# Optimization experiments

Measured on AMD Instinct MI355X. Metric: run time of the kernel, lower is better.

## Reference

```python
import jax, jax.numpy as jnp
import numpy as np

DIM = 64
N_EMBED = 512


def setup_inputs() -> dict:
    key = jax.random.key(0)
    k_x, k_e = jax.random.split(key)
    x = jax.random.normal(k_x, (32, 64, 64, DIM), dtype=jnp.float32)
    # codebook buffer: embed has shape [dim, n_embed] as in the torch module
    embed = jax.random.normal(k_e, (DIM, N_EMBED), dtype=jnp.float32)
    return {"x": x, "embed": embed}


def reference(x, embed):
    # x: [B, H, W, dim]; embed: [dim, n_embed]
    dim = embed.shape[0]
    flat = x.reshape(-1, dim)  # [N, dim]
    # squared euclidean distance (same argmin as torch.cdist's euclid dist)
    # d2[n, k] = ||flat[n]||^2 - 2 flat[n].embed[:,k] + ||embed[:,k]||^2
    d2 = (
        jnp.sum(flat * flat, axis=1, keepdims=True)
        - 2.0 * (flat @ embed)
        + jnp.sum(embed * embed, axis=0)[None, :]
    )  # [N, n_embed]
    embed_ind = jnp.argmin(d2, axis=1)  # [N]
    embed_ind = embed_ind.reshape(x.shape[:-1])  # [B, H, W]
    # embedding lookup from embed.T ([n_embed, dim])
    quantize = jnp.take(embed.T, embed_ind, axis=0)  # [B, H, W, dim]
    diff = jnp.mean(jnp.square(jax.lax.stop_gradient(quantize) - x))
    # straight-through estimator
    quantize_st = x + jax.lax.stop_gradient(quantize - x)
    return quantize_st, diff, embed_ind
```

## Files before the change

kernel.cpp:

```cpp
#include <hip/hip_runtime.h>


#define DIM      64
#define NCODE    512
#define NVEC     (32 * 64 * 64)
#define WAVES    4
#define BLK      256
#define NCT      16
#define CHUNK_DW 3072

typedef unsigned int u32;
typedef __attribute__((ext_vector_type(8)))  short bf16x8;
typedef __attribute__((ext_vector_type(16))) float f32x16;

__device__ __forceinline__ void split3(float v, u32& h, u32& m, u32& lo) {
    const u32 u = __float_as_uint(v);
    h = u >> 16;
    const float r1 = v - __uint_as_float(u & 0xFFFF0000u);
    const u32 u1 = __float_as_uint(r1);
    m = u1 >> 16;
    const float r2 = r1 - __uint_as_float(u1 & 0xFFFF0000u);
    lo = __float_as_uint(r2) >> 16;
}

__global__ void vq_prep(const float* __restrict__ embed,
                        u32* __restrict__ bfrag,
                        float* __restrict__ et,
                        float* __restrict__ norms,
                        float* __restrict__ out) {
    const int gid = blockIdx.x * BLK + threadIdx.x;
    const int c = gid >> 3, g = gid & 7;
    const int s = g >> 1, kh = g & 1;

    float v[8];
    double ns = 0.0;
    #pragma unroll
    for (int j = 0; j < 8; ++j) {
        v[j] = embed[(16 * s + 8 * kh + j) * NCODE + c];
        ns += (double)v[j] * (double)v[j];
    }
    ns += __shfl_xor(ns, 1, 64);
    ns += __shfl_xor(ns, 2, 64);
    ns += __shfl_xor(ns, 4, 64);
    if (g == 0) norms[c] = (float)ns;

    u32 wH[4], wM[4], wL[4];
    #pragma unroll
    for (int q = 0; q < 4; ++q) {
        u32 h0, m0, l0, h1, m1, l1;
        split3(v[2 * q],     h0, m0, l0);
        split3(v[2 * q + 1], h1, m1, l1);
        wH[q] = h0 | (h1 << 16);
        wM[q] = m0 | (m1 << 16);
        wL[q] = l0 | (l1 << 16);
    }
    const int ct = c >> 5, lb = (c & 31) + 32 * kh;
    u32* base = bfrag + ct * CHUNK_DW;
    *reinterpret_cast<uint4*>(base + (0 * 4 + s) * 256 + lb * 4) =
        make_uint4(wH[0], wH[1], wH[2], wH[3]);
    *reinterpret_cast<uint4*>(base + (1 * 4 + s) * 256 + lb * 4) =
        make_uint4(wM[0], wM[1], wM[2], wM[3]);
    *reinterpret_cast<uint4*>(base + (2 * 4 + s) * 256 + lb * 4) =
        make_uint4(wL[0], wL[1], wL[2], wL[3]);

    float* ep = et + c * DIM + 16 * s + 8 * kh;
    *reinterpret_cast<float4*>(ep)     = make_float4(v[0], v[1], v[2], v[3]);
    *reinterpret_cast<float4*>(ep + 4) = make_float4(v[4], v[5], v[6], v[7]);

    if (gid == 0) out[(size_t)NVEC * DIM] = 0.0f;
}

__global__ __launch_bounds__(BLK, 3) void vq_main(
        const float* __restrict__ x,
        const u32* __restrict__ bfrag,
        const float* __restrict__ et,
        const float* __restrict__ norms,
        float* __restrict__ out) {
    __shared__ int sbk[WAVES][32];
    __shared__ float red[WAVES];

    const int tid = threadIdx.x;
    const int wid = tid >> 6, l = tid & 63;
    const int rl = l & 31, kh = l >> 5;
    const int n0 = (blockIdx.x * WAVES + wid) * 32;

    bf16x8 afr[3][4];
    {
        const float* xp = x + (size_t)(n0 + rl) * DIM + kh * 8;
        #pragma unroll
        for (int s = 0; s < 4; ++s) {
            const float4 va = *reinterpret_cast<const float4*>(xp + 16 * s);
            const float4 vb = *reinterpret_cast<const float4*>(xp + 16 * s + 4);
            const float v[8] = {va.x, va.y, va.z, va.w, vb.x, vb.y, vb.z, vb.w};
            #pragma unroll
            for (int q = 0; q < 4; ++q) {
                u32 h0, m0, l0, h1, m1, l1;
                split3(v[2 * q],     h0, m0, l0);
                split3(v[2 * q + 1], h1, m1, l1);
                afr[0][s][2 * q] = (short)h0;  afr[0][s][2 * q + 1] = (short)h1;
                afr[1][s][2 * q] = (short)m0;  afr[1][s][2 * q + 1] = (short)m1;
                afr[2][s][2 * q] = (short)l0;  afr[2][s][2 * q + 1] = (short)l1;
            }
        }
    }

    float best[16];
    int bk[16];
    #pragma unroll
    for (int r = 0; r < 16; ++r) { best[r] = __builtin_inff(); bk[r] = 0; }

    const u32* fb = bfrag + (l << 2);
    for (int ct = 0; ct < NCT; ++ct) {
        const u32* tb = fb + ct * CHUNK_DW;
        bf16x8 b[3][4];
        #pragma unroll
        for (int s = 0; s < 4; ++s) {
            b[0][s] = *reinterpret_cast<const bf16x8*>(tb + (0 * 4 + s) * 256);
            b[1][s] = *reinterpret_cast<const bf16x8*>(tb + (1 * 4 + s) * 256);
            b[2][s] = *reinterpret_cast<const bf16x8*>(tb + (2 * 4 + s) * 256);
        }
        const float nrm = norms[ct * 32 + rl];

        f32x16 acc;
        #pragma unroll
        for (int r = 0; r < 16; ++r) acc[r] = 0.0f;

        #pragma unroll
        for (int s = 0; s < 4; ++s) {
            acc = __builtin_amdgcn_mfma_f32_32x32x16_bf16(afr[0][s], b[0][s], acc, 0, 0, 0);
            acc = __builtin_amdgcn_mfma_f32_32x32x16_bf16(afr[0][s], b[1][s], acc, 0, 0, 0);
            acc = __builtin_amdgcn_mfma_f32_32x32x16_bf16(afr[1][s], b[0][s], acc, 0, 0, 0);
            acc = __builtin_amdgcn_mfma_f32_32x32x16_bf16(afr[1][s], b[1][s], acc, 0, 0, 0);
            acc = __builtin_amdgcn_mfma_f32_32x32x16_bf16(afr[0][s], b[2][s], acc, 0, 0, 0);
            acc = __builtin_amdgcn_mfma_f32_32x32x16_bf16(afr[2][s], b[0][s], acc, 0, 0, 0);
        }

        const int col = ct * 32 + rl;
        #pragma unroll
        for (int r = 0; r < 16; ++r) {
            const float sc = fmaf(-2.0f, acc[r], nrm);
            if (sc < best[r]) { best[r] = sc; bk[r] = col; }
        }
    }

    #pragma unroll
    for (int off = 1; off <= 16; off <<= 1) {
        #pragma unroll
        for (int r = 0; r < 16; ++r) {
            const float ob = __shfl_xor(best[r], off, 64);
            const int obk  = __shfl_xor(bk[r], off, 64);
            if (ob < best[r] || (ob == best[r] && obk < bk[r])) { best[r] = ob; bk[r] = obk; }
        }
    }
    if (rl == 0) {
        #pragma unroll
        for (int r = 0; r < 16; ++r) sbk[wid][(r & 3) + 8 * (r >> 2) + 4 * kh] = bk[r];
    }

    float dp = 0.0f;
    const int rsub = l >> 4;
    const int dcol = (l & 15) * 4;
    #pragma unroll
    for (int i = 0; i < 8; ++i) {
        const int row = i * 4 + rsub;
        const int k = sbk[wid][row];
        const float4 q  = *reinterpret_cast<const float4*>(et + k * DIM + dcol);
        const float4 xv = *reinterpret_cast<const float4*>(x + (size_t)(n0 + row) * DIM + dcol);
        *reinterpret_cast<float4*>(out + (size_t)(n0 + row) * DIM + dcol) = q;
        const float d0 = q.x - xv.x, d1 = q.y - xv.y, d2 = q.z - xv.z, d3 = q.w - xv.w;
        dp = fmaf(d0, d0, dp); dp = fmaf(d1, d1, dp);
        dp = fmaf(d2, d2, dp); dp = fmaf(d3, d3, dp);
    }
    if (l < 32) out[(size_t)NVEC * DIM + 1 + n0 + l] = (float)sbk[wid][l];

    #pragma unroll
    for (int off = 32; off >= 1; off >>= 1) dp += __shfl_down(dp, off, 64);
    if (l == 0) red[wid] = dp;
    __syncthreads();
    if (tid == 0) {
        const float s = (red[0] + red[1]) + (red[2] + red[3]);
        atomicAdd(out + (size_t)NVEC * DIM, s * (1.0f / ((float)NVEC * (float)DIM)));
    }
}

extern "C" void kernel_launch(void* const* d_in, const int* in_sizes, int n_in,
                              void* d_out, int out_size, void* d_ws, size_t ws_size,
                              hipStream_t stream) {
    const float* x     = (const float*)d_in[0];
    const float* embed = (const float*)d_in[1];
    float* out = (float*)d_out;

    u32* bfrag   = (u32*)d_ws;
    float* et    = (float*)d_ws + NCT * CHUNK_DW;
    float* norms = et + (size_t)NCODE * DIM;

    vq_prep<<<16, BLK, 0, stream>>>(embed, bfrag, et, norms, out);
    vq_main<<<NVEC / (WAVES * 32), BLK, 0, stream>>>(x, bfrag, et, norms, out);
}
```

Before: 145.5 us.

## Double-buffer codebook fragment loads across tiles and preload norms

The codebook tile loop is fully unrolled with two register buffers, so the next tile's B fragments are fetched from global memory while MFMAs run on the current tile. Sched barriers pin this ordering and setprio raises priority around the MFMA bursts. All 16 norm values are hoisted into registers before the loop. The extra registers force launch bounds down from 3 to 2 blocks per SM, trading occupancy for hiding load latency within each wave.

```diff
diff --git a/kernel.cpp b/kernel.cpp
--- a/kernel.cpp
+++ b/kernel.cpp
@@ -70,7 +70,36 @@
     if (gid == 0) out[(size_t)NVEC * DIM] = 0.0f;
 }
 
-__global__ __launch_bounds__(BLK, 3) void vq_main(
+#define TILE_MFMA(bset, acc)                                                       \
+    _Pragma("unroll")                                                              \
+    for (int s = 0; s < 4; ++s) {                                                  \
+        acc = __builtin_amdgcn_mfma_f32_32x32x16_bf16(afr[0][s], bset[0 + s], acc, 0, 0, 0); \
+        acc = __builtin_amdgcn_mfma_f32_32x32x16_bf16(afr[0][s], bset[4 + s], acc, 0, 0, 0); \
+        acc = __builtin_amdgcn_mfma_f32_32x32x16_bf16(afr[1][s], bset[0 + s], acc, 0, 0, 0); \
+        acc = __builtin_amdgcn_mfma_f32_32x32x16_bf16(afr[1][s], bset[4 + s], acc, 0, 0, 0); \
+        acc = __builtin_amdgcn_mfma_f32_32x32x16_bf16(afr[0][s], bset[8 + s], acc, 0, 0, 0); \
+        acc = __builtin_amdgcn_mfma_f32_32x32x16_bf16(afr[2][s], bset[0 + s], acc, 0, 0, 0); \
+    }
+
+#define LOAD_SET(dst, tile)                                                        \
+    {                                                                              \
+        const u32* tb_ = fb + (tile) * CHUNK_DW;                                   \
+        _Pragma("unroll")                                                          \
+        for (int j = 0; j < 12; ++j)                                               \
+            dst[j] = *reinterpret_cast<const bf16x8*>(tb_ + j * 256);              \
+    }
+
+#define ARGMIN_UPDATE(acc, ct)                                                     \
+    {                                                                              \
+        const int col_ = (ct) * 32 + rl;                                           \
+        _Pragma("unroll")                                                          \
+        for (int r = 0; r < 16; ++r) {                                             \
+            const float sc_ = fmaf(-2.0f, acc[r], nrm[ct]);                        \
+            if (sc_ < best[r]) { best[r] = sc_; bk[r] = col_; }                    \
+        }                                                                          \
+    }
+
+__global__ __launch_bounds__(BLK, 2) void vq_main(
         const float* __restrict__ x,
         const u32* __restrict__ bfrag,
         const float* __restrict__ et,
@@ -83,6 +112,10 @@
     const int wid = tid >> 6, l = tid & 63;
     const int rl = l & 31, kh = l >> 5;
     const int n0 = (blockIdx.x * WAVES + wid) * 32;
+
+    float nrm[NCT];
+    #pragma unroll
+    for (int ct = 0; ct < NCT; ++ct) nrm[ct] = norms[ct * 32 + rl];
 
     bf16x8 afr[3][4];
     {
@@ -110,37 +143,40 @@
     for (int r = 0; r < 16; ++r) { best[r] = __builtin_inff(); bk[r] = 0; }
 
     const u32* fb = bfrag + (l << 2);
-    for (int ct = 0; ct < NCT; ++ct) {
-        const u32* tb = fb + ct * CHUNK_DW;
-        bf16x8 b[3][4];
-        #pragma unroll
-        for (int s = 0; s < 4; ++s) {
-            b[0][s] = *reinterpret_cast<const bf16x8*>(tb + (0 * 4 + s) * 256);
-            b[1][s] = *reinterpret_cast<const bf16x8*>(tb + (1 * 4 + s) * 256);
-            b[2][s] = *reinterpret_cast<const bf16x8*>(tb + (2 * 4 + s) * 256);
-        }
-        const float nrm = norms[ct * 32 + rl];
-
-        f32x16 acc;
-        #pragma unroll
-        for (int r = 0; r < 16; ++r) acc[r] = 0.0f;
-
-        #pragma unroll
-        for (int s = 0; s < 4; ++s) {
-            acc = __builtin_amdgcn_mfma_f32_32x32x16_bf16(afr[0][s], b[0][s], acc, 0, 0, 0);
-            acc = __builtin_amdgcn_mfma_f32_32x32x16_bf16(afr[0][s], b[1][s], acc, 0, 0, 0);
-            acc = __builtin_amdgcn_mfma_f32_32x32x16_bf16(afr[1][s], b[0][s], acc, 0, 0, 0);
-            acc = __builtin_amdgcn_mfma_f32_32x32x16_bf16(afr[1][s], b[1][s], acc, 0, 0, 0);
-            acc = __builtin_amdgcn_mfma_f32_32x32x16_bf16(afr[0][s], b[2][s], acc, 0, 0, 0);
-            acc = __builtin_amdgcn_mfma_f32_32x32x16_bf16(afr[2][s], b[0][s], acc, 0, 0, 0);
-        }
-
-        const int col = ct * 32 + rl;
-        #pragma unroll
-        for (int r = 0; r < 16; ++r) {
-            const float sc = fmaf(-2.0f, acc[r], nrm);
-            if (sc < best[r]) { best[r] = sc; bk[r] = col; }
-        }
+    bf16x8 s0[12], s1[12];
+
+    LOAD_SET(s0, 0)
+    __builtin_amdgcn_sched_barrier(0);
+
+    #pragma unroll
+    for (int p = 0; p < 8; ++p) {
+        LOAD_SET(s1, 2 * p + 1)
+        __builtin_amdgcn_sched_barrier(0);
+        {
+            f32x16 acc;
+            #pragma unroll
+            for (int r = 0; r < 16; ++r) acc[r] = 0.0f;
+            __builtin_amdgcn_s_setprio(1);
+            TILE_MFMA(s0, acc)
+            __builtin_amdgcn_s_setprio(0);
+            ARGMIN_UPDATE(acc, 2 * p)
+        }
+        __builtin_amdgcn_sched_barrier(0);
+
+        if (p < 7) {
+            LOAD_SET(s0, 2 * p + 2)
+        }
+        __builtin_amdgcn_sched_barrier(0);
+        {
+            f32x16 acc;
+            #pragma unroll
+            for (int r = 0; r < 16; ++r) acc[r] = 0.0f;
+            __builtin_amdgcn_s_setprio(1);
+            TILE_MFMA(s1, acc)
+            __builtin_amdgcn_s_setprio(0);
+            ARGMIN_UPDATE(acc, 2 * p + 1)
+        }
+        __builtin_amdgcn_sched_barrier(0);
     }
 
     #pragma unroll
```

New measurement: 141.6 us. 1.03x faster.
